# Optimization experiments

Measured on AMD Instinct MI355X. Metric: run time of the kernel, lower is better.

The kernel has to match this reference:

```python
import jax, jax.numpy as jnp
import numpy as np

T, D, H, O = 16384, 512, 1024, 512


def setup_inputs() -> dict:
    key = jax.random.key(0)
    k_in, k_h0, kU, kW, kV = jax.random.split(key, 5)
    inputs = jax.random.randint(k_in, (T,), 0, D)
    h0 = jax.random.normal(k_h0, (H,), dtype=jnp.float32)
    U = jax.random.normal(kU, (H, D), dtype=jnp.float32) * 0.01
    W = jax.random.normal(kW, (H, H), dtype=jnp.float32) * 0.01
    V = jax.random.normal(kV, (O, H), dtype=jnp.float32) * 0.01
    bh = jnp.zeros((H,), dtype=jnp.float32)
    by = jnp.zeros((O,), dtype=jnp.float32)
    return {"inputs": inputs, "h0": h0, "U": U, "W": W, "V": V, "bh": bh, "by": by}


def reference(inputs, h0, U, W, V, bh, by):
    # U @ one_hot(x_t) is just a column gather of U; precompute for all t: (T, H)
    Ux = U.T[inputs]

    def step(h, ux):
        h = jnp.tanh(ux + W @ h + bh)  # (H,)
        return h, h

    h_T, hs = jax.lax.scan(step, h0, Ux)  # hs: (T, H)
    logits = hs @ V.T + by  # (T, O)
    return logits, h_T
```

## Files before the change

### kernel.cpp

```cpp
#include <hip/hip_runtime.h>
#include <cstdint>


constexpr int T_STEPS = 16384;
constexpr int D_DIM   = 512;
constexpr int H_DIM   = 1024;
constexpr int O_DIM   = 512;
constexpr int NGRID   = 256;
constexpr int NWORK   = 32;
constexpr int NTHR    = 512;

__device__ __forceinline__ float fast_tanh(float x) {
    float e = __expf(2.f * x);
    return 1.f - 2.f / (e + 1.f);
}
__device__ __forceinline__ float hsum4(const float4& v) {
    return (v.x + v.y) + (v.z + v.w);
}

__device__ __forceinline__ float2 acquire_pair(
    const volatile unsigned long long* fp,
    const unsigned long long* sp, unsigned want)
{
    unsigned long long a, b;
    int k = 0;
    for (;;) {
        if ((k++ & 7) != 7) {
            a = fp[0];
            b = fp[1];
        } else {
            a = __hip_atomic_load(sp + 0, __ATOMIC_RELAXED, __HIP_MEMORY_SCOPE_AGENT);
            b = __hip_atomic_load(sp + 1, __ATOMIC_RELAXED, __HIP_MEMORY_SCOPE_AGENT);
        }
        if ((unsigned)(a >> 32) == want && (unsigned)(b >> 32) == want) break;
    }
    return make_float2(__uint_as_float((unsigned)a), __uint_as_float((unsigned)b));
}

__device__ __forceinline__ void publish(volatile unsigned long long* Fd,
                                        unsigned long long* Sd,
                                        unsigned long long pk)
{
    *Fd = pk;
    __hip_atomic_store(Sd, pk, __ATOMIC_RELAXED, __HIP_MEMORY_SCOPE_AGENT);
}

__global__ __launch_bounds__(NTHR, 2)
void rnn_fused(const int* __restrict__ xs, const float* __restrict__ h0,
               const float* __restrict__ U, const float* __restrict__ W,
               const float* __restrict__ V, const float* __restrict__ bh,
               const float* __restrict__ by, float* __restrict__ out,
               int* __restrict__ ctrl,
               unsigned long long* __restrict__ htagF,
               unsigned long long* __restrict__ htagS)
{
    const int tid = threadIdx.x;

    __shared__ int s_slice;
    if (tid == 0) {
        int xcd;
        asm volatile("s_getreg_b32 %0, hwreg(HW_REG_XCC_ID)" : "=s"(xcd));
        xcd &= 7;
        const int r = __hip_atomic_fetch_add(&ctrl[1 + xcd], 1,
                                             __ATOMIC_RELAXED, __HIP_MEMORY_SCOPE_AGENT);
        if (r == NWORK - 1) {
            int expected = 0;
            __hip_atomic_compare_exchange_strong(&ctrl[0], &expected, xcd + 1,
                __ATOMIC_RELAXED, __ATOMIC_RELAXED, __HIP_MEMORY_SCOPE_AGENT);
        }
        int ch;
        do {
            ch = __hip_atomic_load(&ctrl[0], __ATOMIC_RELAXED, __HIP_MEMORY_SCOPE_AGENT);
        } while (ch == 0);
        s_slice = (ch - 1 == xcd && r < NWORK) ? r : -1;
    }
    __syncthreads();
    const int b = s_slice;
    if (b < 0) return;

    const int w = tid >> 6;
    const int l = tid & 63;

    __shared__ float hl[2][H_DIM];

    const int wr0 = b * 32 + w * 4;
    float4 wreg[4][4];
#pragma unroll
    for (int j = 0; j < 4; ++j)
#pragma unroll
        for (int q = 0; q < 4; ++q)
            wreg[j][q] = *(const float4*)(W + (size_t)(wr0 + j) * H_DIM + 16 * l + 4 * q);
    const float bh_r = bh[wr0 + (l & 3)];
    const int   urow = wr0 + (l & 3);

    const int vr0 = b * 16 + w * 2;
    float4 vreg[2][4];
#pragma unroll
    for (int m = 0; m < 2; ++m)
#pragma unroll
        for (int q = 0; q < 4; ++q)
            vreg[m][q] = *(const float4*)(V + (size_t)(vr0 + m) * H_DIM + 16 * l + 4 * q);
    const float by_r = by[vr0 + (l & 1)];

    int rdw[4];
#pragma unroll
    for (int q = 0; q < 4; ++q)
        rdw[q] = 16 * l + 4 * (q ^ ((l >> 1) & 3));
    const int c   = tid >> 3;
    const int qw  = (tid >> 1) & 3;
    const int wdw = 16 * c + 4 * (qw ^ ((c >> 1) & 3)) + 2 * (tid & 1);

    const bool o1 = (l & 1) != 0, o2 = (l & 2) != 0;

    for (int t = 0; t < T_STEPS; ++t) {
        const int sb = (~t) & 1;
        float* hb = hl[sb];

        const int   xt = xs[t];
        const float uv = U[(size_t)urow * D_DIM + xt];

        float2 hpair;
        if (t == 0) {
            hpair = *(const float2*)(h0 + 2 * tid);
        } else {
            const size_t off = (size_t)((t - 1) & 1) * H_DIM + 2 * tid;
            hpair = acquire_pair(htagF + off, htagS + off, (unsigned)(t - 1));
        }
        *(float2*)&hb[wdw] = hpair;
        __syncthreads();

        float4 h4[4];
#pragma unroll
        for (int q = 0; q < 4; ++q) h4[q] = *(const float4*)&hb[rdw[q]];

        float s[4];
#pragma unroll
        for (int j = 0; j < 4; ++j) {
            float4 a = make_float4(0.f, 0.f, 0.f, 0.f);
#pragma unroll
            for (int q = 0; q < 4; ++q) {
                a.x += wreg[j][q].x * h4[q].x;
                a.y += wreg[j][q].y * h4[q].y;
                a.z += wreg[j][q].z * h4[q].z;
                a.w += wreg[j][q].w * h4[q].w;
            }
            s[j] = hsum4(a);
        }
        float A  = o1 ? s[1] : s[0], Ax = o1 ? s[0] : s[1];
        float B  = o1 ? s[3] : s[2], Bx = o1 ? s[2] : s[3];
        A += __shfl_xor(Ax, 1);
        B += __shfl_xor(Bx, 1);
        float Cv = o2 ? B : A, Cx = o2 ? A : B;
        Cv += __shfl_xor(Cx, 2);
        Cv += __shfl_xor(Cv, 4);
        Cv += __shfl_xor(Cv, 8);
        Cv += __shfl_xor(Cv, 16);
        Cv += __shfl_xor(Cv, 32);

        const float hv = fast_tanh(Cv + bh_r + uv);
        if (l < 4) {
            const unsigned long long pk =
                ((unsigned long long)(unsigned)t << 32) | (unsigned long long)__float_as_uint(hv);
            const size_t doff = (size_t)(t & 1) * H_DIM + wr0 + l;
            publish(htagF + doff, htagS + doff, pk);
        }

        if (t > 0) {
            float sv[2];
#pragma unroll
            for (int m = 0; m < 2; ++m) {
                float4 a = make_float4(0.f, 0.f, 0.f, 0.f);
#pragma unroll
                for (int q = 0; q < 4; ++q) {
                    a.x += vreg[m][q].x * h4[q].x;
                    a.y += vreg[m][q].y * h4[q].y;
                    a.z += vreg[m][q].z * h4[q].z;
                    a.w += vreg[m][q].w * h4[q].w;
                }
                sv[m] = hsum4(a);
            }
            float P  = o1 ? sv[1] : sv[0], Px = o1 ? sv[0] : sv[1];
            P += __shfl_xor(Px, 1);
            P += __shfl_xor(P, 2);
            P += __shfl_xor(P, 4);
            P += __shfl_xor(P, 8);
            P += __shfl_xor(P, 16);
            P += __shfl_xor(P, 32);
            if (l < 2) out[(size_t)(t - 1) * O_DIM + vr0 + l] = P + by_r;
        }
    }

    {
        const size_t off = (size_t)((T_STEPS - 1) & 1) * H_DIM + 2 * tid;
        float2 hpair = acquire_pair(htagF + off, htagS + off, (unsigned)(T_STEPS - 1));
        if (b == 0)
            *(float2*)&out[(size_t)T_STEPS * O_DIM + 2 * tid] = hpair;

        float* hb = hl[1];
        *(float2*)&hb[wdw] = hpair;
        __syncthreads();
        float4 h4[4];
#pragma unroll
        for (int q = 0; q < 4; ++q) h4[q] = *(const float4*)&hb[rdw[q]];
        float sv[2];
#pragma unroll
        for (int m = 0; m < 2; ++m) {
            float4 a = make_float4(0.f, 0.f, 0.f, 0.f);
#pragma unroll
            for (int q = 0; q < 4; ++q) {
                a.x += vreg[m][q].x * h4[q].x;
                a.y += vreg[m][q].y * h4[q].y;
                a.z += vreg[m][q].z * h4[q].z;
                a.w += vreg[m][q].w * h4[q].w;
            }
            sv[m] = hsum4(a);
        }
        float P  = o1 ? sv[1] : sv[0], Px = o1 ? sv[0] : sv[1];
        P += __shfl_xor(Px, 1);
        P += __shfl_xor(P, 2);
        P += __shfl_xor(P, 4);
        P += __shfl_xor(P, 8);
        P += __shfl_xor(P, 16);
        P += __shfl_xor(P, 32);
        if (l < 2) out[(size_t)(T_STEPS - 1) * O_DIM + vr0 + l] = P + by_r;
    }
}

extern "C" void kernel_launch(void* const* d_in, const int* in_sizes, int n_in,
                              void* d_out, int out_size, void* d_ws, size_t ws_size,
                              hipStream_t stream) {
    const int*   xs = (const int*)d_in[0];
    const float* h0 = (const float*)d_in[1];
    const float* U  = (const float*)d_in[2];
    const float* W  = (const float*)d_in[3];
    const float* V  = (const float*)d_in[4];
    const float* bh = (const float*)d_in[5];
    const float* by = (const float*)d_in[6];
    float* out = (float*)d_out;

    int* ctrl = (int*)d_ws;
    unsigned long long* htagF = (unsigned long long*)((char*)d_ws + 256);
    unsigned long long* htagS = htagF + 2 * H_DIM;

    hipMemsetAsync(d_ws, 0, 256, stream);
    hipMemsetAsync((char*)d_ws + 256, 0xAA,
                   4 * H_DIM * sizeof(unsigned long long), stream);

    rnn_fused<<<NGRID, NTHR, 0, stream>>>(xs, h0, U, W, V, bh, by, out,
                                          ctrl, htagF, htagS);
}
```

Measured before the change: 26.20 ms.

## Use single tagged h buffer with probed fast mode, DPP reductions, packed FMA

Drops the dual volatile/atomic publish buffers in favor of one tagged buffer. A startup handshake checks whether all 32 worker blocks see each other's volatile writes, then picks plain volatile polling (fast mode) or agent-scope atomics for every step. The per-row reductions change from butterfly shuffles to DPP row and broadcast adds with packed v2f FMAs, and a single lane now computes tanh for four rows and publishes them. Intended to shorten the per-step critical path of the serial recurrence. The visibility probe is a heuristic: relying on volatile coherence across CUs could hang if it is wrong.

```diff
diff --git a/kernel.cpp b/kernel.cpp
--- a/kernel.cpp
+++ b/kernel.cpp
@@ -10,39 +10,26 @@
 constexpr int NWORK   = 32;
 constexpr int NTHR    = 512;
 
+typedef float v2f __attribute__((ext_vector_type(2)));
+
 __device__ __forceinline__ float fast_tanh(float x) {
     float e = __expf(2.f * x);
     return 1.f - 2.f / (e + 1.f);
 }
-__device__ __forceinline__ float hsum4(const float4& v) {
-    return (v.x + v.y) + (v.z + v.w);
-}
-
-__device__ __forceinline__ float2 acquire_pair(
-    const volatile unsigned long long* fp,
-    const unsigned long long* sp, unsigned want)
-{
-    unsigned long long a, b;
-    int k = 0;
-    for (;;) {
-        if ((k++ & 7) != 7) {
-            a = fp[0];
-            b = fp[1];
-        } else {
-            a = __hip_atomic_load(sp + 0, __ATOMIC_RELAXED, __HIP_MEMORY_SCOPE_AGENT);
-            b = __hip_atomic_load(sp + 1, __ATOMIC_RELAXED, __HIP_MEMORY_SCOPE_AGENT);
-        }
-        if ((unsigned)(a >> 32) == want && (unsigned)(b >> 32) == want) break;
-    }
-    return make_float2(__uint_as_float((unsigned)a), __uint_as_float((unsigned)b));
-}
-
-__device__ __forceinline__ void publish(volatile unsigned long long* Fd,
-                                        unsigned long long* Sd,
-                                        unsigned long long pk)
-{
-    *Fd = pk;
-    __hip_atomic_store(Sd, pk, __ATOMIC_RELAXED, __HIP_MEMORY_SCOPE_AGENT);
+
+template<int CTRL>
+__device__ __forceinline__ float dpp_add(float x) {
+    int m = __builtin_amdgcn_update_dpp(0, __float_as_int(x), CTRL, 0xf, 0xf, true);
+    return x + __int_as_float(m);
+}
+__device__ __forceinline__ float wave_sum_dpp(float x) {
+    x = dpp_add<0x111>(x);
+    x = dpp_add<0x112>(x);
+    x = dpp_add<0x114>(x);
+    x = dpp_add<0x118>(x);
+    x = dpp_add<0x142>(x);
+    x = dpp_add<0x143>(x);
+    return x;
 }
 
 __global__ __launch_bounds__(NTHR, 2)
@@ -50,13 +37,11 @@
                const float* __restrict__ U, const float* __restrict__ W,
                const float* __restrict__ V, const float* __restrict__ bh,
                const float* __restrict__ by, float* __restrict__ out,
-               int* __restrict__ ctrl,
-               unsigned long long* __restrict__ htagF,
-               unsigned long long* __restrict__ htagS)
+               int* __restrict__ ctrl, unsigned long long* __restrict__ htag)
 {
     const int tid = threadIdx.x;
 
-    __shared__ int s_slice;
+    __shared__ int s_slice, s_mode;
     if (tid == 0) {
         int xcd;
         asm volatile("s_getreg_b32 %0, hwreg(HW_REG_XCC_ID)" : "=s"(xcd));
@@ -72,11 +57,34 @@
         do {
             ch = __hip_atomic_load(&ctrl[0], __ATOMIC_RELAXED, __HIP_MEMORY_SCOPE_AGENT);
         } while (ch == 0);
-        s_slice = (ch - 1 == xcd && r < NWORK) ? r : -1;
+        const int slice = (ch - 1 == xcd && r < NWORK) ? r : -1;
+        s_slice = slice;
+
+        int mode = 0;
+        if (slice >= 0) {
+            ((volatile int*)ctrl)[16 + slice] = 0x5EED0000 | slice;
+            if (slice == 0) {
+                mode = 1;
+                for (int pass = 0; pass < (1 << 17); ++pass) {
+                    bool all = true;
+                    for (int rr = 0; rr < NWORK; ++rr)
+                        if (((volatile int*)ctrl)[16 + rr] != (0x5EED0000 | rr)) { all = false; break; }
+                    if (all) break;
+                    if (pass == (1 << 17) - 1) mode = 2;
+                }
+                __hip_atomic_store(&ctrl[9], mode, __ATOMIC_RELAXED, __HIP_MEMORY_SCOPE_AGENT);
+            } else {
+                do {
+                    mode = __hip_atomic_load(&ctrl[9], __ATOMIC_RELAXED, __HIP_MEMORY_SCOPE_AGENT);
+                } while (mode == 0);
+            }
+        }
+        s_mode = mode;
     }
     __syncthreads();
     const int b = s_slice;
     if (b < 0) return;
+    const bool fast = (s_mode == 1);
 
     const int w = tid >> 6;
     const int l = tid & 63;
@@ -84,23 +92,22 @@
     __shared__ float hl[2][H_DIM];
 
     const int wr0 = b * 32 + w * 4;
-    float4 wreg[4][4];
+    v2f wreg[4][8];
 #pragma unroll
     for (int j = 0; j < 4; ++j)
 #pragma unroll
-        for (int q = 0; q < 4; ++q)
-            wreg[j][q] = *(const float4*)(W + (size_t)(wr0 + j) * H_DIM + 16 * l + 4 * q);
-    const float bh_r = bh[wr0 + (l & 3)];
-    const int   urow = wr0 + (l & 3);
+        for (int q = 0; q < 8; ++q)
+            wreg[j][q] = *(const v2f*)(W + (size_t)(wr0 + j) * H_DIM + 16 * l + 2 * q);
+    const float4 bh4 = *(const float4*)(bh + wr0);
 
     const int vr0 = b * 16 + w * 2;
-    float4 vreg[2][4];
+    v2f vreg[2][8];
 #pragma unroll
     for (int m = 0; m < 2; ++m)
 #pragma unroll
-        for (int q = 0; q < 4; ++q)
-            vreg[m][q] = *(const float4*)(V + (size_t)(vr0 + m) * H_DIM + 16 * l + 4 * q);
-    const float by_r = by[vr0 + (l & 1)];
+        for (int q = 0; q < 8; ++q)
+            vreg[m][q] = *(const v2f*)(V + (size_t)(vr0 + m) * H_DIM + 16 * l + 2 * q);
+    const float2 by2 = *(const float2*)(by + vr0);
 
     int rdw[4];
 #pragma unroll
@@ -110,21 +117,40 @@
     const int qw  = (tid >> 1) & 3;
     const int wdw = 16 * c + 4 * (qw ^ ((c >> 1) & 3)) + 2 * (tid & 1);
 
-    const bool o1 = (l & 1) != 0, o2 = (l & 2) != 0;
+    const bool pub = (l == 63);
 
     for (int t = 0; t < T_STEPS; ++t) {
         const int sb = (~t) & 1;
         float* hb = hl[sb];
 
-        const int   xt = xs[t];
-        const float uv = U[(size_t)urow * D_DIM + xt];
+        const int xt = xs[t];
+        float u0 = 0.f, u1 = 0.f, u2 = 0.f, u3 = 0.f;
+        if (pub) {
+            u0 = U[(size_t)(wr0 + 0) * D_DIM + xt];
+            u1 = U[(size_t)(wr0 + 1) * D_DIM + xt];
+            u2 = U[(size_t)(wr0 + 2) * D_DIM + xt];
+            u3 = U[(size_t)(wr0 + 3) * D_DIM + xt];
+        }
 
         float2 hpair;
         if (t == 0) {
             hpair = *(const float2*)(h0 + 2 * tid);
         } else {
             const size_t off = (size_t)((t - 1) & 1) * H_DIM + 2 * tid;
-            hpair = acquire_pair(htagF + off, htagS + off, (unsigned)(t - 1));
+            const unsigned want = (unsigned)(t - 1);
+            unsigned long long a, bq;
+            if (fast) {
+                const volatile unsigned long long* fp = htag + off;
+                do { a = fp[0]; bq = fp[1]; }
+                while ((unsigned)(a >> 32) != want || (unsigned)(bq >> 32) != want);
+            } else {
+                const unsigned long long* sp = htag + off;
+                do {
+                    a  = __hip_atomic_load(sp + 0, __ATOMIC_RELAXED, __HIP_MEMORY_SCOPE_AGENT);
+                    bq = __hip_atomic_load(sp + 1, __ATOMIC_RELAXED, __HIP_MEMORY_SCOPE_AGENT);
+                } while ((unsigned)(a >> 32) != want || (unsigned)(bq >> 32) != want);
+            }
+            hpair = make_float2(__uint_as_float((unsigned)a), __uint_as_float((unsigned)bq));
         }
         *(float2*)&hb[wdw] = hpair;
         __syncthreads();
@@ -132,67 +158,88 @@
         float4 h4[4];
 #pragma unroll
         for (int q = 0; q < 4; ++q) h4[q] = *(const float4*)&hb[rdw[q]];
-
-        float s[4];
-#pragma unroll
-        for (int j = 0; j < 4; ++j) {
-            float4 a = make_float4(0.f, 0.f, 0.f, 0.f);
-#pragma unroll
-            for (int q = 0; q < 4; ++q) {
-                a.x += wreg[j][q].x * h4[q].x;
-                a.y += wreg[j][q].y * h4[q].y;
-                a.z += wreg[j][q].z * h4[q].z;
-                a.w += wreg[j][q].w * h4[q].w;
-            }
-            s[j] = hsum4(a);
-        }
-        float A  = o1 ? s[1] : s[0], Ax = o1 ? s[0] : s[1];
-        float B  = o1 ? s[3] : s[2], Bx = o1 ? s[2] : s[3];
-        A += __shfl_xor(Ax, 1);
-        B += __shfl_xor(Bx, 1);
-        float Cv = o2 ? B : A, Cx = o2 ? A : B;
-        Cv += __shfl_xor(Cx, 2);
-        Cv += __shfl_xor(Cv, 4);
-        Cv += __shfl_xor(Cv, 8);
-        Cv += __shfl_xor(Cv, 16);
-        Cv += __shfl_xor(Cv, 32);
-
-        const float hv = fast_tanh(Cv + bh_r + uv);
-        if (l < 4) {
-            const unsigned long long pk =
-                ((unsigned long long)(unsigned)t << 32) | (unsigned long long)__float_as_uint(hv);
-            const size_t doff = (size_t)(t & 1) * H_DIM + wr0 + l;
-            publish(htagF + doff, htagS + doff, pk);
+        v2f h2[8];
+#pragma unroll
+        for (int q = 0; q < 4; ++q) {
+            h2[2 * q]     = v2f{h4[q].x, h4[q].y};
+            h2[2 * q + 1] = v2f{h4[q].z, h4[q].w};
+        }
+
+        float s0, s1, s2, s3;
+        {
+            v2f a[4];
+#pragma unroll
+            for (int j = 0; j < 4; ++j) {
+                v2f e = v2f{0.f, 0.f}, o = v2f{0.f, 0.f};
+#pragma unroll
+                for (int q = 0; q < 4; ++q) {
+                    e = __builtin_elementwise_fma(wreg[j][2 * q],     h2[2 * q],     e);
+                    o = __builtin_elementwise_fma(wreg[j][2 * q + 1], h2[2 * q + 1], o);
+                }
+                a[j] = e + o;
+            }
+            s0 = a[0].x + a[0].y; s1 = a[1].x + a[1].y;
+            s2 = a[2].x + a[2].y; s3 = a[3].x + a[3].y;
+        }
+        s0 = wave_sum_dpp(s0);
+        s1 = wave_sum_dpp(s1);
+        s2 = wave_sum_dpp(s2);
+        s3 = wave_sum_dpp(s3);
+
+        if (pub) {
+            const unsigned long long hi = (unsigned long long)(unsigned)t << 32;
+            unsigned long long p0 = hi | __float_as_uint(fast_tanh(s0 + bh4.x + u0));
+            unsigned long long p1 = hi | __float_as_uint(fast_tanh(s1 + bh4.y + u1));
+            unsigned long long p2 = hi | __float_as_uint(fast_tanh(s2 + bh4.z + u2));
+            unsigned long long p3 = hi | __float_as_uint(fast_tanh(s3 + bh4.w + u3));
+            unsigned long long* dst = htag + (size_t)(t & 1) * H_DIM + wr0;
+            if (fast) {
+                volatile unsigned long long* fd = dst;
+                fd[0] = p0; fd[1] = p1; fd[2] = p2; fd[3] = p3;
+            } else {
+                __hip_atomic_store(dst + 0, p0, __ATOMIC_RELAXED, __HIP_MEMORY_SCOPE_AGENT);
+                __hip_atomic_store(dst + 1, p1, __ATOMIC_RELAXED, __HIP_MEMORY_SCOPE_AGENT);
+                __hip_atomic_store(dst + 2, p2, __ATOMIC_RELAXED, __HIP_MEMORY_SCOPE_AGENT);
+                __hip_atomic_store(dst + 3, p3, __ATOMIC_RELAXED, __HIP_MEMORY_SCOPE_AGENT);
+            }
         }
 
         if (t > 0) {
-            float sv[2];
-#pragma unroll
-            for (int m = 0; m < 2; ++m) {
-                float4 a = make_float4(0.f, 0.f, 0.f, 0.f);
-#pragma unroll
-                for (int q = 0; q < 4; ++q) {
-                    a.x += vreg[m][q].x * h4[q].x;
-                    a.y += vreg[m][q].y * h4[q].y;
-                    a.z += vreg[m][q].z * h4[q].z;
-                    a.w += vreg[m][q].w * h4[q].w;
+            float sv0, sv1;
+            {
+                v2f e0 = v2f{0.f, 0.f}, e1 = v2f{0.f, 0.f};
+#pragma unroll
+                for (int q = 0; q < 8; ++q) {
+                    e0 = __builtin_elementwise_fma(vreg[0][q], h2[q], e0);
+                    e1 = __builtin_elementwise_fma(vreg[1][q], h2[q], e1);
                 }
-                sv[m] = hsum4(a);
-            }
-            float P  = o1 ? sv[1] : sv[0], Px = o1 ? sv[0] : sv[1];
-            P += __shfl_xor(Px, 1);
-            P += __shfl_xor(P, 2);
-            P += __shfl_xor(P, 4);
-            P += __shfl_xor(P, 8);
-            P += __shfl_xor(P, 16);
-            P += __shfl_xor(P, 32);
-            if (l < 2) out[(size_t)(t - 1) * O_DIM + vr0 + l] = P + by_r;
+                sv0 = e0.x + e0.y; sv1 = e1.x + e1.y;
+            }
+            sv0 = wave_sum_dpp(sv0);
+            sv1 = wave_sum_dpp(sv1);
+            if (pub)
+                *(float2*)&out[(size_t)(t - 1) * O_DIM + vr0] =
+                    make_float2(sv0 + by2.x, sv1 + by2.y);
         }
     }
 
     {
         const size_t off = (size_t)((T_STEPS - 1) & 1) * H_DIM + 2 * tid;
-        float2 hpair = acquire_pair(htagF + off, htagS + off, (unsigned)(T_STEPS - 1));
+        const unsigned want = (unsigned)(T_STEPS - 1);
+        unsigned long long a, bq;
+        if (fast) {
+            const volatile unsigned long long* fp = htag + off;
+            do { a = fp[0]; bq = fp[1]; }
+            while ((unsigned)(a >> 32) != want || (unsigned)(bq >> 32) != want);
+        } else {
+            const unsigned long long* sp = htag + off;
+            do {
+                a  = __hip_atomic_load(sp + 0, __ATOMIC_RELAXED, __HIP_MEMORY_SCOPE_AGENT);
+                bq = __hip_atomic_load(sp + 1, __ATOMIC_RELAXED, __HIP_MEMORY_SCOPE_AGENT);
+            } while ((unsigned)(a >> 32) != want || (unsigned)(bq >> 32) != want);
+        }
+        float2 hpair = make_float2(__uint_as_float((unsigned)a),
+                                   __uint_as_float((unsigned)bq));
         if (b == 0)
             *(float2*)&out[(size_t)T_STEPS * O_DIM + 2 * tid] = hpair;
 
@@ -202,27 +249,23 @@
         float4 h4[4];
 #pragma unroll
         for (int q = 0; q < 4; ++q) h4[q] = *(const float4*)&hb[rdw[q]];
-        float sv[2];
-#pragma unroll
-        for (int m = 0; m < 2; ++m) {
-            float4 a = make_float4(0.f, 0.f, 0.f, 0.f);
-#pragma unroll
-            for (int q = 0; q < 4; ++q) {
-                a.x += vreg[m][q].x * h4[q].x;
-                a.y += vreg[m][q].y * h4[q].y;
-                a.z += vreg[m][q].z * h4[q].z;
-                a.w += vreg[m][q].w * h4[q].w;
-            }
-            sv[m] = hsum4(a);
-        }
-        float P  = o1 ? sv[1] : sv[0], Px = o1 ? sv[0] : sv[1];
-        P += __shfl_xor(Px, 1);
-        P += __shfl_xor(P, 2);
-        P += __shfl_xor(P, 4);
-        P += __shfl_xor(P, 8);
-        P += __shfl_xor(P, 16);
-        P += __shfl_xor(P, 32);
-        if (l < 2) out[(size_t)(T_STEPS - 1) * O_DIM + vr0 + l] = P + by_r;
+        v2f h2[8];
+#pragma unroll
+        for (int q = 0; q < 4; ++q) {
+            h2[2 * q]     = v2f{h4[q].x, h4[q].y};
+            h2[2 * q + 1] = v2f{h4[q].z, h4[q].w};
+        }
+        v2f e0 = v2f{0.f, 0.f}, e1 = v2f{0.f, 0.f};
+#pragma unroll
+        for (int q = 0; q < 8; ++q) {
+            e0 = __builtin_elementwise_fma(vreg[0][q], h2[q], e0);
+            e1 = __builtin_elementwise_fma(vreg[1][q], h2[q], e1);
+        }
+        float sv0 = wave_sum_dpp(e0.x + e0.y);
+        float sv1 = wave_sum_dpp(e1.x + e1.y);
+        if (pub)
+            *(float2*)&out[(size_t)(T_STEPS - 1) * O_DIM + vr0] =
+                make_float2(sv0 + by2.x, sv1 + by2.y);
     }
 }
 
@@ -239,13 +282,11 @@
     float* out = (float*)d_out;
 
     int* ctrl = (int*)d_ws;
-    unsigned long long* htagF = (unsigned long long*)((char*)d_ws + 256);
-    unsigned long long* htagS = htagF + 2 * H_DIM;
+    unsigned long long* htag = (unsigned long long*)((char*)d_ws + 256);
 
     hipMemsetAsync(d_ws, 0, 256, stream);
     hipMemsetAsync((char*)d_ws + 256, 0xAA,
-                   4 * H_DIM * sizeof(unsigned long long), stream);
-
-    rnn_fused<<<NGRID, NTHR, 0, stream>>>(xs, h0, U, W, V, bh, by, out,
-                                          ctrl, htagF, htagS);
-}
+                   2 * H_DIM * sizeof(unsigned long long), stream);
+
+    rnn_fused<<<NGRID, NTHR, 0, stream>>>(xs, h0, U, W, V, bh, by, out, ctrl, htag);
+}
```

Result: slower. 53.19 ms (+103.0%).
